# Performance work log

Measured on AMD Instinct MI355X. Metric: run time of the kernel, lower is better.

## Reference

```python
import jax, jax.numpy as jnp
import numpy as np

D_MODEL = 768
HEADS = 12
D_HEAD = D_MODEL // HEADS
D_DYNA = 768
EPS = 1e-5
B, SP, SI = 16, 256, 1024


def _layernorm(x, g, b):
    mu = jnp.mean(x, axis=-1, keepdims=True)
    var = jnp.var(x, axis=-1, keepdims=True)
    return (x - mu) * jax.lax.rsqrt(var + EPS) * g + b


def _mha(q, k, v, wq, bq, wk, bk, wv, bv, wo, bo):
    # weights stored [d_in, d_out]; torch Linear math y = x @ W^T + b is
    # equivalent with transposed storage.
    B_ = q.shape[0]
    qh = (q @ wq + bq).reshape(B_, -1, HEADS, D_HEAD)
    kh = (k @ wk + bk).reshape(B_, -1, HEADS, D_HEAD)
    vh = (v @ wv + bv).reshape(B_, -1, HEADS, D_HEAD)
    scores = jnp.einsum('bqhd,bkhd->bhqk', qh, kh) / np.sqrt(D_HEAD).astype(np.float32)
    attn = jax.nn.softmax(scores, axis=-1)  # dropout disabled (eval)
    out = jnp.einsum('bhqk,bkhd->bqhd', attn, vh).reshape(B_, -1, D_MODEL)
    return out @ wo + bo


def setup_inputs() -> dict:
    key = jax.random.key(0)
    ks = iter(jax.random.split(key, 40))
    s = 0.02
    d = {
        'image': jax.random.normal(next(ks), (B, SI, D_MODEL), jnp.float32),
        'prompt': jax.random.normal(next(ks), (B, SP, D_MODEL), jnp.float32),
        'posi': jax.random.normal(next(ks), (B, SI, D_MODEL), jnp.float32),
        'posp': jax.random.normal(next(ks), (B, SP, D_MODEL), jnp.float32),
    }
    for ln in ('ln_p1', 'ln_p2', 'ln_p3', 'ln_i1'):
        d[ln + '_g'] = jnp.ones((D_MODEL,), jnp.float32)
        d[ln + '_b'] = jnp.zeros((D_MODEL,), jnp.float32)
    for pre in ('pp', 'pi'):
        for nm in ('q', 'k', 'v', 'o'):
            d[f'{pre}_w{nm}'] = s * jax.random.normal(next(ks), (D_MODEL, D_MODEL), jnp.float32)
            d[f'{pre}_b{nm}'] = jnp.zeros((D_MODEL,), jnp.float32)
    d['ff_w1'] = s * jax.random.normal(next(ks), (D_MODEL, D_MODEL), jnp.float32)
    d['ff_b1'] = jnp.zeros((D_MODEL,), jnp.float32)
    d['ff_w2'] = s * jax.random.normal(next(ks), (D_MODEL, D_DYNA), jnp.float32)
    d['ff_b2'] = jnp.zeros((D_DYNA,), jnp.float32)
    return d


def reference(image, prompt, posi, posp,
              ln_p1_g, ln_p1_b, ln_p2_g, ln_p2_b, ln_p3_g, ln_p3_b, ln_i1_g, ln_i1_b,
              pp_wq, pp_bq, pp_wk, pp_bk, pp_wv, pp_bv, pp_wo, pp_bo,
              pi_wq, pi_bq, pi_wk, pi_bk, pi_wv, pi_bv, pi_wo, pi_bo,
              ff_w1, ff_b1, ff_w2, ff_b2):
    prompt0 = prompt + posp
    xp = _layernorm(prompt0, ln_p1_g, ln_p1_b)
    xp = _mha(xp, xp, xp, pp_wq, pp_bq, pp_wk, pp_bk, pp_wv, pp_bv, pp_wo, pp_bo)
    prompt = prompt + xp  # dropout_p1 is identity in eval
    xp = _layernorm(prompt + prompt0, ln_p2_g, ln_p2_b)
    xi = _layernorm(image + posi, ln_i1_g, ln_i1_b)
    xp = _mha(xp, xi, xi, pi_wq, pi_bq, pi_wk, pi_bk, pi_wv, pi_bv, pi_wo, pi_bo)
    prompt = prompt + xp  # dropout_p2 identity
    xp = _layernorm(prompt + prompt0, ln_p3_g, ln_p3_b)
    xp = jax.nn.relu(xp @ ff_w1 + ff_b1) @ ff_w2 + ff_b2
    return xp
```

## Files before the change

### kernel.cpp

```cpp
#include <hip/hip_runtime.h>
#include <hip/hip_bf16.h>
#include <stdint.h>
#include <math.h>

#define D_MODEL 768
#define HEADS 12
#define D_HEAD 64
#define BATCH 16
#define SP 256
#define SI 1024
#define NP (BATCH * SP)
#define NI (BATCH * SI)

#define GLOBAL_AS __attribute__((address_space(1)))
#define LDS_AS    __attribute__((address_space(3)))

typedef __attribute__((ext_vector_type(8))) short  frag_ab;
typedef __attribute__((ext_vector_type(4))) float  frag_cd;

static __device__ __forceinline__ ushort f2bf(float f) {
  __hip_bfloat16 h = __float2bfloat16(f);
  return *(ushort*)&h;
}
static __device__ __forceinline__ float bf2f(ushort u) {
  return __bfloat162float(*(__hip_bfloat16*)&u);
}
static __device__ __forceinline__ bool probe_bf(const uint32_t* p) {
  return p[0] == 0x3F803F80u;
}

struct Prep {
  const void* wsrc[10]; ushort* wdst[10];
  const void* vsrc[18]; float* vdst;
};

__global__ __launch_bounds__(256) void prep_kernel(Prep p, const uint32_t* probe) {
  const bool isbf = probe_bf(probe);
  const int z = blockIdx.z;
  if (z < 10) {
    __shared__ float tile[32][33];
    const int tx = threadIdx.x & 31, ty = threadIdx.x >> 5;
    const int x0 = blockIdx.x * 32, y0 = blockIdx.y * 32;
    const void* src = p.wsrc[z];
    ushort* dst = p.wdst[z];
#pragma unroll
    for (int i = 0; i < 4; i++) {
      const int y = y0 + ty + i * 8;
      float v;
      if (isbf) v = bf2f(((const ushort*)src)[(size_t)y * 768 + x0 + tx]);
      else      v = ((const float*)src)[(size_t)y * 768 + x0 + tx];
      tile[ty + i * 8][tx] = v;
    }
    __syncthreads();
#pragma unroll
    for (int i = 0; i < 4; i++) {
      const int row = x0 + ty + i * 8;
      const int col = y0 + tx;
      dst[(size_t)row * 768 + col] = f2bf(tile[tx][ty + i * 8]);
    }
  } else {
    const int idx = (blockIdx.y * 24 + blockIdx.x) * 256 + threadIdx.x;
    if (idx < 18 * 768) {
      const int e = idx / 768, i = idx - e * 768;
      float v;
      if (isbf) v = bf2f(((const ushort*)p.vsrc[e])[i]);
      else      v = ((const float*)p.vsrc[e])[i];
      p.vdst[idx] = v;
    }
  }
}

struct LNJob {
  const void* a; const void* b;
  const float* g; const float* be;
  float* sum_out; ushort* ln_out;
  int nrows; int abf;
};

__global__ __launch_bounds__(192) void add_ln2(LNJob J0, LNJob J1, const uint32_t* probe) {
  int row = blockIdx.x;
  LNJob j = (row < J0.nrows) ? J0 : J1;
  if (row >= J0.nrows) row -= J0.nrows;
  const int tid = threadIdx.x;
  const size_t base = (size_t)row * D_MODEL;
  const int c0 = tid * 4;
  const bool isbf = j.abf && probe_bf(probe);
  float x[4];
  if (isbf) {
    const uint2 ua = *(const uint2*)((const ushort*)j.a + base + c0);
    const uint2 ub = *(const uint2*)((const ushort*)j.b + base + c0);
    const ushort* pa = (const ushort*)&ua;
    const ushort* pb = (const ushort*)&ub;
#pragma unroll
    for (int t = 0; t < 4; t++) x[t] = bf2f(pa[t]) + bf2f(pb[t]);
  } else {
    const float4 fa = *(const float4*)((const float*)j.a + base + c0);
    const float4 fb = *(const float4*)((const float*)j.b + base + c0);
    x[0] = fa.x + fb.x; x[1] = fa.y + fb.y; x[2] = fa.z + fb.z; x[3] = fa.w + fb.w;
  }
  if (j.sum_out) {
    float4 s4; s4.x = x[0]; s4.y = x[1]; s4.z = x[2]; s4.w = x[3];
    *(float4*)&j.sum_out[base + c0] = s4;
  }
  __shared__ float rs[192], rq[192];
  __shared__ float stats[2];
  rs[tid] = x[0] + x[1] + x[2] + x[3];
  rq[tid] = x[0]*x[0] + x[1]*x[1] + x[2]*x[2] + x[3]*x[3];
  __syncthreads();
  if (tid < 64) {
    float s = rs[tid] + rs[tid + 64] + rs[tid + 128];
    float q = rq[tid] + rq[tid + 64] + rq[tid + 128];
#pragma unroll
    for (int o = 32; o > 0; o >>= 1) { s += __shfl_down(s, o); q += __shfl_down(q, o); }
    if (tid == 0) {
      const float mu  = s * (1.0f / D_MODEL);
      const float var = q * (1.0f / D_MODEL) - mu * mu;
      stats[0] = mu;
      stats[1] = rsqrtf(var + 1e-5f);
    }
  }
  __syncthreads();
  const float mu = stats[0], inv = stats[1];
  const float4 gv = *(const float4*)&j.g[c0];
  const float4 bv = *(const float4*)&j.be[c0];
  uint2 ou;
  ushort* oe = (ushort*)&ou;
  oe[0] = f2bf((x[0] - mu) * inv * gv.x + bv.x);
  oe[1] = f2bf((x[1] - mu) * inv * gv.y + bv.y);
  oe[2] = f2bf((x[2] - mu) * inv * gv.z + bv.z);
  oe[3] = f2bf((x[3] - mu) * inv * gv.w + bv.w);
  *(uint2*)(j.ln_out + base + c0) = ou;
}

template<int BM>
__global__ __launch_bounds__(256) void gemm_k(
    const ushort* __restrict__ A, const ushort* __restrict__ Bt,
    const float* __restrict__ bias,
    const void* __restrict__ resid, int rmode,
    void* __restrict__ C, int relu, int omode,
    const uint32_t* __restrict__ probe, int X) {
  __shared__ ushort As[BM * 32];
  __shared__ ushort Bs[128 * 32];
  const int tid  = threadIdx.x;
  const int lane = tid & 63, w = tid >> 6;
  const int wr = w >> 1, wc = w & 1;
  const int ml = lane & 15, kq = lane >> 4;
  const int bid = blockIdx.x;
  const int rest = bid >> 3;
  const int x = rest % X, y = (bid & 7) + 8 * (rest / X);
  const int m0 = y * BM, n0 = x * 128;
  constexpr int MT   = BM / 32;
  constexpr int ASEG = BM / 16;
  constexpr int NSEG = (ASEG + 8) / 4;

  frag_cd acc[MT][4] = {};

  for (int k0 = 0; k0 < 768; k0 += 32) {
#pragma unroll
    for (int i = 0; i < NSEG; i++) {
      const int s = w + i * 4;
      const bool isA = (s < ASEG);
      const int seg = isA ? s : (s - ASEG);
      const int r   = seg * 16 + (lane >> 2);
      const int kof = k0 + (lane & 3) * 8;
      if (isA)
        __builtin_amdgcn_global_load_lds((const GLOBAL_AS void*)(A + (size_t)(m0 + r) * 768 + kof),
            (LDS_AS void*)((LDS_AS ushort*)As + seg * 512), 16, 0, 0);
      else
        __builtin_amdgcn_global_load_lds((const GLOBAL_AS void*)(Bt + (size_t)(n0 + r) * 768 + kof),
            (LDS_AS void*)((LDS_AS ushort*)Bs + seg * 512), 16, 0, 0);
    }
    __syncthreads();

    frag_ab af[MT], bf4[4];
#pragma unroll
    for (int t = 0; t < MT; t++)
      af[t] = *(const frag_ab*)&As[(wr * (BM / 2) + t * 16 + ml) * 32 + kq * 8];
#pragma unroll
    for (int t = 0; t < 4; t++)
      bf4[t] = *(const frag_ab*)&Bs[(wc * 64 + t * 16 + ml) * 32 + kq * 8];
#pragma unroll
    for (int mt = 0; mt < MT; mt++)
#pragma unroll
      for (int nt = 0; nt < 4; nt++)
        acc[mt][nt] = __builtin_amdgcn_mfma_f32_16x16x32_bf16(
            af[mt], bf4[nt], acc[mt][nt], 0, 0, 0);
    __syncthreads();
  }

  const bool obf = (omode == 1) || (omode == 2 && probe_bf(probe));
  const bool rbf = (rmode == 2) && probe_bf(probe);
#pragma unroll
  for (int mt = 0; mt < MT; mt++) {
#pragma unroll
    for (int nt = 0; nt < 4; nt++) {
      const int row0 = m0 + wr * (BM / 2) + mt * 16 + kq * 4;
      const int col  = n0 + wc * 64 + nt * 16 + ml;
      const float bc = bias[col];
#pragma unroll
      for (int r = 0; r < 4; r++) {
        const size_t off = (size_t)(row0 + r) * 768 + col;
        float v = acc[mt][nt][r] + bc;
        if (rmode != 0)
          v += rbf ? bf2f(((const ushort*)resid)[off]) : ((const float*)resid)[off];
        if (relu) v = fmaxf(v, 0.f);
        if (obf) ((ushort*)C)[off] = f2bf(v);
        else     ((float*)C)[off]  = v;
      }
    }
  }
}

struct GJob {
  const ushort* A; const ushort* Bt; const float* bias;
  ushort* o0; ushort* o1; ushort* vT;
  int X; int vsub; int shift;
};

__global__ __launch_bounds__(256) void gemm_mega(GJob J0, GJob J1, int n0blocks) {
  __shared__ ushort As[128 * 32];
  __shared__ ushort Bs[128 * 32];
  int bid = blockIdx.x;
  GJob j = (bid < n0blocks) ? J0 : J1;
  if (bid >= n0blocks) bid -= n0blocks;
  const int tid  = threadIdx.x;
  const int lane = tid & 63, w = tid >> 6;
  const int wr = w >> 1, wc = w & 1;
  const int ml = lane & 15, kq = lane >> 4;
  const int rest = bid >> 3;
  const int x = rest % j.X, y = (bid & 7) + 8 * (rest / j.X);
  const int m0 = y * 128, n0 = x * 128;

  frag_cd acc[4][4] = {};

  for (int k0 = 0; k0 < 768; k0 += 32) {
#pragma unroll
    for (int i = 0; i < 2; i++) {
      const int seg = w * 2 + i;
      const int r   = seg * 16 + (lane >> 2);
      const int kof = k0 + (lane & 3) * 8;
      __builtin_amdgcn_global_load_lds((const GLOBAL_AS void*)(j.A + (size_t)(m0 + r) * 768 + kof),
          (LDS_AS void*)((LDS_AS ushort*)As + seg * 512), 16, 0, 0);
      __builtin_amdgcn_global_load_lds((const GLOBAL_AS void*)(j.Bt + (size_t)(n0 + r) * 768 + kof),
          (LDS_AS void*)((LDS_AS ushort*)Bs + seg * 512), 16, 0, 0);
    }
    __syncthreads();

    frag_ab af[4], bf4[4];
#pragma unroll
    for (int t = 0; t < 4; t++) {
      af[t]  = *(const frag_ab*)&As[(wr * 64 + t * 16 + ml) * 32 + kq * 8];
      bf4[t] = *(const frag_ab*)&Bs[(wc * 64 + t * 16 + ml) * 32 + kq * 8];
    }
#pragma unroll
    for (int mt = 0; mt < 4; mt++)
#pragma unroll
      for (int nt = 0; nt < 4; nt++)
        acc[mt][nt] = __builtin_amdgcn_mfma_f32_16x16x32_bf16(
            af[mt], bf4[nt], acc[mt][nt], 0, 0, 0);
    __syncthreads();
  }

  const int sub  = x / 6;
  const int mask = (1 << j.shift) - 1;
#pragma unroll
  for (int mt = 0; mt < 4; mt++) {
#pragma unroll
    for (int nt = 0; nt < 4; nt++) {
      const int row0 = m0 + wr * 64 + mt * 16 + kq * 4;
      const int col  = n0 + wc * 64 + nt * 16 + ml;
      const float bc = j.bias[col];
      if (sub == j.vsub) {
        const int hcol = col - sub * 768;
        const int hh = hcol >> 6, dd = hcol & 63;
        const int bb = row0 >> j.shift;
        const int jj = row0 & mask;
        uint2 pack;
        ushort* pe = (ushort*)&pack;
#pragma unroll
        for (int r = 0; r < 4; r++) pe[r] = f2bf(acc[mt][nt][r] + bc);
        *(uint2*)(j.vT + ((((size_t)(bb * HEADS + hh) << 6) + dd) << j.shift) + jj) = pack;
      } else {
        ushort* out = (sub == 0) ? j.o0 : j.o1;
        const int cl = col - sub * 768;
#pragma unroll
        for (int r = 0; r < 4; r++)
          out[(size_t)(row0 + r) * 768 + cl] = f2bf(acc[mt][nt][r] + bc);
      }
    }
  }
}

#define FS 68
__global__ __launch_bounds__(256) void fattn_mfma(
    const ushort* __restrict__ Q, const ushort* __restrict__ Kp,
    const ushort* __restrict__ vT, ushort* __restrict__ O, int Skv) {
  __shared__ __align__(16) ushort Qs[64 * FS];
  __shared__ __align__(16) ushort Ks[64 * FS];
  __shared__ __align__(16) ushort Vt[64 * FS];
  __shared__ __align__(16) ushort Ps[64 * FS];
  const int tid  = threadIdx.x;
  const int lane = tid & 63, w = tid >> 6;
  const int ml   = lane & 15, kq = lane >> 4;
  const int bid = blockIdx.x;
  const int g8  = bid & 7;
  const int qt  = (bid >> 3) & 3;
  const int g   = (bid >> 5) * 8 + g8;
  const int h   = g % HEADS;
  const int b   = g / HEADS;
  const int q0  = qt * 64;
  const ushort* Qb  = Q  + ((size_t)b * SP + q0) * D_MODEL + h * D_HEAD;
  const ushort* Kb  = Kp + (size_t)b * Skv * D_MODEL + h * D_HEAD;
  const ushort* vTb = vT + (size_t)g * 64 * Skv;

  for (int c = tid; c < 512; c += 256) {
    const int r = c >> 3, p = c & 7;
    *(uint4*)&Qs[r * FS + p * 8] = *(const uint4*)(Qb + (size_t)r * D_MODEL + p * 8);
  }
  __syncthreads();
  frag_ab qa[2];
#pragma unroll
  for (int kc = 0; kc < 2; kc++)
    qa[kc] = *(const frag_ab*)&Qs[(w * 16 + ml) * FS + kc * 32 + kq * 8];

  frag_cd oc[4] = {};
  float m_i[4], l_i[4];
#pragma unroll
  for (int r = 0; r < 4; r++) { m_i[r] = -1e30f; l_i[r] = 0.f; }
  const float SCL = 0.125f * 1.44269504f;

  for (int j0 = 0; j0 < Skv; j0 += 64) {
    __syncthreads();
    for (int c = tid; c < 512; c += 256) {
      const int r = c >> 3, p = c & 7;
      *(uint4*)&Ks[r * FS + p * 8] = *(const uint4*)(Kb + (size_t)(j0 + r) * D_MODEL + p * 8);
      *(uint4*)&Vt[r * FS + p * 8] = *(const uint4*)(vTb + (size_t)r * Skv + j0 + p * 8);
    }
    __syncthreads();

    frag_cd sc[4] = {};
#pragma unroll
    for (int nt = 0; nt < 4; nt++)
#pragma unroll
      for (int kc = 0; kc < 2; kc++) {
        const frag_ab bfr = *(const frag_ab*)&Ks[(nt * 16 + ml) * FS + kc * 32 + kq * 8];
        sc[nt] = __builtin_amdgcn_mfma_f32_16x16x32_bf16(qa[kc], bfr, sc[nt], 0, 0, 0);
      }
#pragma unroll
    for (int nt = 0; nt < 4; nt++)
#pragma unroll
      for (int r = 0; r < 4; r++) sc[nt][r] *= SCL;

    float al[4];
#pragma unroll
    for (int r = 0; r < 4; r++) {
      float mx = fmaxf(fmaxf(sc[0][r], sc[1][r]), fmaxf(sc[2][r], sc[3][r]));
#pragma unroll
      for (int m = 1; m < 16; m <<= 1) mx = fmaxf(mx, __shfl_xor(mx, m, 16));
      const float mnew = fmaxf(m_i[r], mx);
      al[r] = exp2f(m_i[r] - mnew);
      float p[4], s = 0.f;
#pragma unroll
      for (int nt = 0; nt < 4; nt++) { p[nt] = exp2f(sc[nt][r] - mnew); s += p[nt]; }
#pragma unroll
      for (int m = 1; m < 16; m <<= 1) s += __shfl_xor(s, m, 16);
      l_i[r] = l_i[r] * al[r] + s;
      m_i[r] = mnew;
      const int prow = (w * 16 + kq * 4 + r) * FS;
#pragma unroll
      for (int nt = 0; nt < 4; nt++) Ps[prow + nt * 16 + ml] = f2bf(p[nt]);
    }
#pragma unroll
    for (int dt = 0; dt < 4; dt++)
#pragma unroll
      for (int r = 0; r < 4; r++) oc[dt][r] *= al[r];

#pragma unroll
    for (int kc = 0; kc < 2; kc++) {
      const frag_ab pa = *(const frag_ab*)&Ps[(w * 16 + ml) * FS + kc * 32 + kq * 8];
#pragma unroll
      for (int dt = 0; dt < 4; dt++) {
        const frag_ab vb = *(const frag_ab*)&Vt[(dt * 16 + ml) * FS + kc * 32 + kq * 8];
        oc[dt] = __builtin_amdgcn_mfma_f32_16x16x32_bf16(pa, vb, oc[dt], 0, 0, 0);
      }
    }
  }

  float inv[4];
#pragma unroll
  for (int r = 0; r < 4; r++) inv[r] = 1.0f / l_i[r];
#pragma unroll
  for (int dt = 0; dt < 4; dt++)
#pragma unroll
    for (int r = 0; r < 4; r++)
      O[((size_t)b * SP + q0 + w * 16 + kq * 4 + r) * D_MODEL + h * D_HEAD + dt * 16 + ml] =
          f2bf(oc[dt][r] * inv[r]);
}

extern "C" void kernel_launch(void* const* d_in, const int* in_sizes, int n_in,
                              void* d_out, int out_size, void* d_ws, size_t ws_size,
                              hipStream_t stream) {
  (void)in_sizes; (void)n_in; (void)out_size;
  char* base = (char*)d_ws;
  size_t off = 256;
  auto alloc = [&](size_t bytes) -> char* {
    char* p = base + off;
    off = (off + bytes + 255) & ~(size_t)255;
    return p;
  };
  const size_t WB = (size_t)768 * 768 * 2;
  ushort* Wt[10];
  for (int i = 0; i < 10; i++) Wt[i] = (ushort*)alloc(WB);
  float* vecs = (float*)alloc(18 * 768 * 4);
  float* biasF[10];
  for (int i = 0; i < 10; i++) biasF[i] = vecs + i * 768;
  float* lnF = vecs + 10 * 768;
  float* prompt0 = (float*)alloc((size_t)NP * 768 * 4);
  float* cur     = (float*)alloc((size_t)NP * 768 * 4);
  ushort* q_bf   = (ushort*)alloc((size_t)NP * 768 * 2);
  ushort* k_s    = (ushort*)alloc((size_t)NP * 768 * 2);
  ushort* k_c    = (ushort*)alloc((size_t)NI * 768 * 2);
  ushort* xln_bf = (ushort*)alloc((size_t)NP * 768 * 2);
  ushort* xi_bf  = (ushort*)alloc((size_t)NI * 768 * 2);
  ushort* obuf_bf = (ushort*)alloc((size_t)NP * 768 * 2);
  ushort* ffn1_bf = (ushort*)alloc((size_t)NP * 768 * 2);
  ushort* vT_s   = (ushort*)alloc((size_t)BATCH * HEADS * 64 * SP * 2);
  ushort* vT_c   = (ushort*)alloc((size_t)BATCH * HEADS * 64 * SI * 2);
  if (ws_size < off) return;

  const uint32_t* probe = (const uint32_t*)d_in[4];
  const int widx[10] = {12, 14, 16, 18, 20, 22, 24, 26, 28, 30};
  const int bidx[10] = {13, 15, 17, 19, 21, 23, 25, 27, 29, 31};

  Prep pr{};
  for (int i = 0; i < 10; i++) { pr.wsrc[i] = d_in[widx[i]]; pr.wdst[i] = Wt[i]; }
  for (int i = 0; i < 10; i++) pr.vsrc[i] = d_in[bidx[i]];
  for (int i = 0; i < 8;  i++) pr.vsrc[10 + i] = d_in[4 + i];
  pr.vdst = vecs;
  prep_kernel<<<dim3(24, 24, 11), 256, 0, stream>>>(pr, probe);

  float* G1 = lnF + 0 * 768, *B1 = lnF + 1 * 768;
  float* G2 = lnF + 2 * 768, *B2 = lnF + 3 * 768;
  float* G3 = lnF + 4 * 768, *B3 = lnF + 5 * 768;
  float* Gi = lnF + 6 * 768, *Bi = lnF + 7 * 768;

  LNJob L0{d_in[1], d_in[3], G1, B1, prompt0, xln_bf, NP, 1};
  LNJob Li{d_in[0], d_in[2], Gi, Bi, nullptr, xi_bf,  NI, 1};
  add_ln2<<<NP + NI, 192, 0, stream>>>(L0, Li, probe);

  GJob js{xln_bf, Wt[0], biasF[0], q_bf, k_s, vT_s, 18, 2, 8};
  GJob jc{xi_bf,  Wt[5], biasF[5], k_c,  nullptr, vT_c, 12, 1, 10};
  gemm_mega<<<576 + 1536, 256, 0, stream>>>(js, jc, 576);

  fattn_mfma<<<BATCH * HEADS * (SP / 64), 256, 0, stream>>>(q_bf, k_s, vT_s, obuf_bf, SP);

  gemm_k<64><<<6 * 64, 256, 0, stream>>>(obuf_bf, Wt[3], biasF[3],
      d_in[1], 2, cur, 0, 0, probe, 6);

  LNJob L2{cur, prompt0, G2, B2, nullptr, xln_bf, NP, 0};
  LNJob Lz{}; Lz.nrows = 0;
  add_ln2<<<NP, 192, 0, stream>>>(L2, Lz, probe);

  gemm_k<64><<<6 * 64, 256, 0, stream>>>(xln_bf, Wt[4], biasF[4],
      nullptr, 0, q_bf, 0, 1, probe, 6);

  fattn_mfma<<<BATCH * HEADS * (SP / 64), 256, 0, stream>>>(q_bf, k_c, vT_c, obuf_bf, SI);

  gemm_k<64><<<6 * 64, 256, 0, stream>>>(obuf_bf, Wt[7], biasF[7],
      cur, 1, cur, 0, 0, probe, 6);

  LNJob L3{cur, prompt0, G3, B3, nullptr, xln_bf, NP, 0};
  add_ln2<<<NP, 192, 0, stream>>>(L3, Lz, probe);

  gemm_k<64><<<6 * 64, 256, 0, stream>>>(xln_bf, Wt[8], biasF[8],
      nullptr, 0, ffn1_bf, 1, 1, probe, 6);

  gemm_k<64><<<6 * 64, 256, 0, stream>>>(ffn1_bf, Wt[9], biasF[9],
      nullptr, 0, d_out, 0, 2, probe, 6);
}
```

Measured before the change: 506.8 us.

## Rewrite fused QKV projection GEMM with 256x256 tiles and double-buffered LDS pipeline

Replaces the 128x128-tile, 32-deep K loop GEMM with a 256x256-tile, 512-thread kernel. It uses 64-wide K stages, double-buffered LDS with an XOR swizzle, interleaved global_load_lds prefetch and MFMA phases, and s_setprio. The aim is to raise arithmetic intensity per loaded byte, avoid LDS bank conflicts, and overlap memory with compute for the large QKV and cross-attention KV projections. In exchange it carries much higher register pressure (acc[8][4] plus fragments) and fewer blocks (528). The hand-scheduled barrier and waitcnt logic is delicate.

```diff
diff --git a/kernel.cpp b/kernel.cpp
--- a/kernel.cpp
+++ b/kernel.cpp
@@ -217,58 +217,130 @@
   int X; int vsub; int shift;
 };
 
-__global__ __launch_bounds__(256) void gemm_mega(GJob J0, GJob J1, int n0blocks) {
-  __shared__ ushort As[128 * 32];
-  __shared__ ushort Bs[128 * 32];
+#define BAR   __builtin_amdgcn_s_barrier()
+#define LGKM0 do { asm volatile("s_waitcnt lgkmcnt(0)" ::: "memory"); \
+                   __builtin_amdgcn_sched_barrier(0); } while (0)
+#define VMC4  do { asm volatile("s_waitcnt vmcnt(4)" ::: "memory"); \
+                   __builtin_amdgcn_sched_barrier(0); } while (0)
+
+#define RD_A(SL, ro) do { \
+  const ushort* _b = &lds[SL][wr][0]; \
+  _Pragma("unroll") for (int _m = 0; _m < 4; ++_m) \
+  _Pragma("unroll") for (int _k = 0; _k < 2; ++_k) \
+    aF[_m][_k] = *(const frag_ab*)(_b + ((ro) + _m * 16 + ml) * 64 + \
+                                   (((_k << 5) + (kq << 3)) ^ swz)); \
+} while (0)
+
+#define RD_B(DST, SL, ro) do { \
+  const ushort* _b = &lds[SL][2 + (wc >> 1)][0]; \
+  _Pragma("unroll") for (int _n = 0; _n < 2; ++_n) \
+  _Pragma("unroll") for (int _k = 0; _k < 2; ++_k) \
+    DST[_n][_k] = *(const frag_ab*)(_b + ((wcl << 6) + (ro) + _n * 16 + ml) * 64 + \
+                                    (((_k << 5) + (kq << 3)) ^ swz)); \
+} while (0)
+
+#define MM(MB, NB, BF) do { \
+  __builtin_amdgcn_s_setprio(1); \
+  _Pragma("unroll") for (int _m = 0; _m < 4; ++_m) \
+  _Pragma("unroll") for (int _n = 0; _n < 2; ++_n) \
+  _Pragma("unroll") for (int _k = 0; _k < 2; ++_k) \
+    acc[(MB) + _m][(NB) + _n] = __builtin_amdgcn_mfma_f32_16x16x32_bf16( \
+        aF[_m][_k], BF[_n][_k], acc[(MB) + _m][(NB) + _n], 0, 0, 0); \
+  __builtin_amdgcn_s_setprio(0); \
+} while (0)
+
+#define STAGE(SL, RG, PTR, RBASE, KT) do { \
+  const ushort* _p = (PTR) + (size_t)((RBASE) + srow) * 768 + ((KT) << 6) + scol; \
+  __builtin_amdgcn_global_load_lds((const GLOBAL_AS void*)_p, \
+      (LDS_AS void*)((LDS_AS ushort*)&lds[SL][RG][0] + (w << 9)), 16, 0, 0); \
+  __builtin_amdgcn_global_load_lds((const GLOBAL_AS void*)(_p + (size_t)64 * 768), \
+      (LDS_AS void*)((LDS_AS ushort*)&lds[SL][RG][0] + 4096 + (w << 9)), 16, 0, 0); \
+} while (0)
+
+__global__ __launch_bounds__(512, 2) void gemm_mega256(GJob J0, GJob J1, int n0blocks) {
+  __shared__ __align__(16) ushort lds[2][4][8192];
   int bid = blockIdx.x;
   GJob j = (bid < n0blocks) ? J0 : J1;
   if (bid >= n0blocks) bid -= n0blocks;
   const int tid  = threadIdx.x;
   const int lane = tid & 63, w = tid >> 6;
-  const int wr = w >> 1, wc = w & 1;
+  const int wr = w >> 2, wc = w & 3, wcl = wc & 1;
   const int ml = lane & 15, kq = lane >> 4;
   const int rest = bid >> 3;
   const int x = rest % j.X, y = (bid & 7) + 8 * (rest / j.X);
-  const int m0 = y * 128, n0 = x * 128;
-
-  frag_cd acc[4][4] = {};
-
-  for (int k0 = 0; k0 < 768; k0 += 32) {
-#pragma unroll
-    for (int i = 0; i < 2; i++) {
-      const int seg = w * 2 + i;
-      const int r   = seg * 16 + (lane >> 2);
-      const int kof = k0 + (lane & 3) * 8;
-      __builtin_amdgcn_global_load_lds((const GLOBAL_AS void*)(j.A + (size_t)(m0 + r) * 768 + kof),
-          (LDS_AS void*)((LDS_AS ushort*)As + seg * 512), 16, 0, 0);
-      __builtin_amdgcn_global_load_lds((const GLOBAL_AS void*)(j.Bt + (size_t)(n0 + r) * 768 + kof),
-          (LDS_AS void*)((LDS_AS ushort*)Bs + seg * 512), 16, 0, 0);
-    }
-    __syncthreads();
-
-    frag_ab af[4], bf4[4];
-#pragma unroll
-    for (int t = 0; t < 4; t++) {
-      af[t]  = *(const frag_ab*)&As[(wr * 64 + t * 16 + ml) * 32 + kq * 8];
-      bf4[t] = *(const frag_ab*)&Bs[(wc * 64 + t * 16 + ml) * 32 + kq * 8];
-    }
-#pragma unroll
-    for (int mt = 0; mt < 4; mt++)
-#pragma unroll
-      for (int nt = 0; nt < 4; nt++)
-        acc[mt][nt] = __builtin_amdgcn_mfma_f32_16x16x32_bf16(
-            af[mt], bf4[nt], acc[mt][nt], 0, 0, 0);
-    __syncthreads();
-  }
-
-  const int sub  = x / 6;
+  const int m0 = y << 8, n0 = x << 8;
+  const int srow = (w << 3) + (lane >> 3);
+  const int scol = (((lane & 7) ^ (lane >> 3)) << 3);
+  const int swz  = (ml & 7) << 3;
+  const ushort* jA = j.A;
+  const ushort* jB = j.Bt;
+
+  frag_cd acc[8][4] = {};
+  frag_ab aF[4][2], bF0[2][2], bF1[2][2];
+
+  STAGE(0, 0, jA, m0, 0);
+  STAGE(0, 1, jA, m0 + 128, 0);
+  STAGE(0, 2, jB, n0, 0);
+  STAGE(0, 3, jB, n0 + 128, 0);
+  STAGE(1, 2, jB, n0, 1);
+  STAGE(1, 3, jB, n0 + 128, 1);
+  VMC4;
+  BAR;
+
+  for (int it = 0; it < 6; ++it) {
+    const int t1  = 2 * it + 1;
+    const int tn0 = (2 * it + 2 < 12) ? 2 * it + 2 : 11;
+    const int tn1 = (2 * it + 3 < 12) ? 2 * it + 3 : 11;
+    RD_A(0, 0); RD_B(bF0, 0, 0);
+    STAGE(1, 0, jA, m0, t1);
+    BAR; LGKM0;
+    MM(0, 0, bF0);
+    BAR;
+    RD_B(bF1, 0, 32);
+    STAGE(1, 1, jA, m0 + 128, t1);
+    BAR; LGKM0;
+    MM(0, 2, bF1);
+    BAR;
+    RD_A(0, 64);
+    STAGE(0, 2, jB, n0, tn0);
+    BAR; LGKM0;
+    MM(4, 2, bF1);
+    BAR;
+    STAGE(0, 3, jB, n0 + 128, tn0);
+    BAR;
+    MM(4, 0, bF0);
+    VMC4;
+    BAR;
+    RD_A(1, 0); RD_B(bF0, 1, 0);
+    STAGE(0, 0, jA, m0, tn0);
+    BAR; LGKM0;
+    MM(0, 0, bF0);
+    BAR;
+    RD_B(bF1, 1, 32);
+    STAGE(0, 1, jA, m0 + 128, tn0);
+    BAR; LGKM0;
+    MM(0, 2, bF1);
+    BAR;
+    RD_A(1, 64);
+    STAGE(1, 2, jB, n0, tn1);
+    BAR; LGKM0;
+    MM(4, 2, bF1);
+    BAR;
+    STAGE(1, 3, jB, n0 + 128, tn1);
+    BAR;
+    MM(4, 0, bF0);
+    VMC4;
+    BAR;
+  }
+
+  const int sub  = x / 3;
   const int mask = (1 << j.shift) - 1;
 #pragma unroll
-  for (int mt = 0; mt < 4; mt++) {
-#pragma unroll
-    for (int nt = 0; nt < 4; nt++) {
-      const int row0 = m0 + wr * 64 + mt * 16 + kq * 4;
-      const int col  = n0 + wc * 64 + nt * 16 + ml;
+  for (int mi = 0; mi < 8; ++mi) {
+#pragma unroll
+    for (int ni = 0; ni < 4; ++ni) {
+      const int row0 = m0 + (wr << 7) + mi * 16 + (kq << 2);
+      const int col  = n0 + (wc << 6) + ni * 16 + ml;
       const float bc = j.bias[col];
       if (sub == j.vsub) {
         const int hcol = col - sub * 768;
@@ -278,18 +350,23 @@
         uint2 pack;
         ushort* pe = (ushort*)&pack;
 #pragma unroll
-        for (int r = 0; r < 4; r++) pe[r] = f2bf(acc[mt][nt][r] + bc);
+        for (int r = 0; r < 4; r++) pe[r] = f2bf(acc[mi][ni][r] + bc);
         *(uint2*)(j.vT + ((((size_t)(bb * HEADS + hh) << 6) + dd) << j.shift) + jj) = pack;
       } else {
         ushort* out = (sub == 0) ? j.o0 : j.o1;
         const int cl = col - sub * 768;
 #pragma unroll
         for (int r = 0; r < 4; r++)
-          out[(size_t)(row0 + r) * 768 + cl] = f2bf(acc[mt][nt][r] + bc);
+          out[(size_t)(row0 + r) * 768 + cl] = f2bf(acc[mi][ni][r] + bc);
       }
     }
   }
 }
+
+#undef RD_A
+#undef RD_B
+#undef MM
+#undef STAGE
 
 #define FS 68
 __global__ __launch_bounds__(256) void fattn_mfma(
@@ -448,9 +525,9 @@
   LNJob Li{d_in[0], d_in[2], Gi, Bi, nullptr, xi_bf,  NI, 1};
   add_ln2<<<NP + NI, 192, 0, stream>>>(L0, Li, probe);
 
-  GJob js{xln_bf, Wt[0], biasF[0], q_bf, k_s, vT_s, 18, 2, 8};
-  GJob jc{xi_bf,  Wt[5], biasF[5], k_c,  nullptr, vT_c, 12, 1, 10};
-  gemm_mega<<<576 + 1536, 256, 0, stream>>>(js, jc, 576);
+  GJob js{xln_bf, Wt[0], biasF[0], q_bf, k_s, vT_s, 9, 2, 8};
+  GJob jc{xi_bf,  Wt[5], biasF[5], k_c,  nullptr, vT_c, 6, 1, 10};
+  gemm_mega256<<<144 + 384, 512, 0, stream>>>(js, jc, 144);
 
   fattn_mfma<<<BATCH * HEADS * (SP / 64), 256, 0, stream>>>(q_bf, k_s, vT_s, obuf_bf, SP);
 
```

Result: no change. 506.9 us (+0.0%).
